# Performance work log

Hardware: AMD Instinct MI355X
Metric: run time of the kernel (lower is better)

Reference implementation:

```python
import jax, jax.numpy as jnp
import numpy as np


def setup_inputs() -> dict:
    key = jax.random.key(0)
    k1, k2 = jax.random.split(key)
    B, C, H, W = 8, 256, 128, 128
    x = jax.random.normal(k1, (B, C, H, W), dtype=jnp.float32)
    # prior plays the role of torch.rand initial selection score (shape [B, H*W])
    prior = jax.random.uniform(k2, (B, H * W), dtype=jnp.float32)
    return {"x": x, "prior": prior, "nbVec": 16}


def reference(x, prior, nbVec):
    # representativeVectors(x, nbVec, prior=prior, onlySimSample=True, applyUMAP=False)
    B, C, H, W = x.shape
    N = H * W
    xf = x.transpose(0, 2, 3, 1).reshape(B, N, C)  # [B, N, C]
    batch = jnp.arange(B)
    EPS = 1e-12  # numerical guard for sqrt at the selected point (dist == 0)

    def step(carry, i):
        score, selpos = carry  # score: [B, N] selection score, selpos: [B, N]
        # i == 0: deterministic center pick; else data-dependent argmax of score
        ind = jnp.where(i == 0, N // 2, jnp.argmax(score, axis=1))  # [B]
        selpos = selpos.at[batch, ind].add(1.0)
        rv = xf[batch, ind]  # gathered representative candidates [B, C]
        # exp(-euclidean_dist / 20) similarity to every spatial position
        d = jnp.sqrt(jnp.sum((xf - rv[:, None, :]) ** 2, axis=-1) + EPS)  # [B, N]
        sim = jnp.exp(-d / 20.0)
        simNorm = sim / jnp.sum(sim, axis=1, keepdims=True)
        repr_vec = jnp.einsum('bnc,bn->bc', xf, simNorm)  # weighted reduction
        score = jnp.where(i == 0, 1.0 - sim, (1.0 - sim) * score)
        return (score, selpos), (repr_vec, sim)

    init = (prior, jnp.zeros((B, N), dtype=x.dtype))
    (_, selpos), (reprVecs, sims) = jax.lax.scan(step, init, jnp.arange(nbVec))
    # reprVecs: [nbVec, B, C]; sims -> [nbVec, B, 1, H, W]; selpos -> [B, 1, H, W]
    return reprVecs, sims.reshape(nbVec, B, 1, H, W), selpos.reshape(B, 1, H, W)
```

## Files before the change

kernel.cpp:

```cpp
#include <hip/hip_runtime.h>
#include <math.h>

#define BB 8
#define CC 256
#define HH 128
#define WW 128
#define NN (HH*WW)
#define NBVEC 16
#define CSPLIT 16
#define CCHUNK (CC/CSPLIT)
#define NBX (NN/256)


__global__ __launch_bounds__(256, 8)
void fused_kernel(const float* __restrict__ x,
                  float* __restrict__ out,
                  const double* __restrict__ bmaxv,
                  const int* __restrict__ bmaxi,
                  double* __restrict__ d2part,
                  double* __restrict__ wpart, int iter)
{
    const int b  = blockIdx.z;
    const int cz = blockIdx.y;
    const int nb = blockIdx.x;
    const int t  = threadIdx.x;
    const int n  = nb*256 + t;

    __shared__ float s_x[CCHUNK][257];
    __shared__ float s_sim[256];
    __shared__ float s_rv[CCHUNK];
    __shared__ union UScratch {
        double part[16][CCHUNK];
        struct { double val[NBX]; int idx[NBX]; } mx;
    } s_u;

    float* out_sims   = out + (size_t)NBVEC*BB*CC;
    float* out_selpos = out_sims + (size_t)NBVEC*BB*NN;

    int sel = NN/2;
    if (iter > 0 && iter < NBVEC) {
        if (t < NBX) { s_u.mx.val[t] = bmaxv[b*NBX + t]; s_u.mx.idx[t] = bmaxi[b*NBX + t]; }
        __syncthreads();
        for (int s = NBX/2; s > 0; s >>= 1) {
            if (t < s) {
                double v2 = s_u.mx.val[t+s]; int i2 = s_u.mx.idx[t+s];
                if (v2 > s_u.mx.val[t] || (v2 == s_u.mx.val[t] && i2 < s_u.mx.idx[t])) {
                    s_u.mx.val[t] = v2; s_u.mx.idx[t] = i2;
                }
            }
            __syncthreads();
        }
        sel = s_u.mx.idx[0];
    }

    if (iter < NBVEC) {
        if (t < CCHUNK)
            s_rv[t] = x[((size_t)b*CC + (size_t)cz*CCHUNK + t)*NN + sel];
        if (t == 0 && nb == 0 && cz == 0)
            out_selpos[(size_t)b*NN + sel] += 1.0f;
    }
    if (iter > 0)
        s_sim[t] = out_sims[(size_t)(iter-1)*BB*NN + (size_t)b*NN + n];
    __syncthreads();

    const float* xb = x + ((size_t)b*CC + (size_t)cz*CCHUNK)*NN;
    float r[CCHUNK];
    #pragma unroll
    for (int c = 0; c < CCHUNK; ++c)
        r[c] = xb[(size_t)c*NN + n];
    #pragma unroll
    for (int c = 0; c < CCHUNK; ++c)
        s_x[c][t] = r[c];

    if (iter < NBVEC) {
        double acc = 0.0;
        #pragma unroll
        for (int c = 0; c < CCHUNK; ++c) {
            double diff = (double)r[c] - (double)s_rv[c];
            acc = fma(diff, diff, acc);
        }
        d2part[((size_t)cz*BB + b)*NN + n] = acc;
    }
    __syncthreads();

    if (iter > 0) {
        const int c = t & 15;
        const int g = t >> 4;
        double w = 0.0;
        #pragma unroll
        for (int k = 0; k < 16; ++k) {
            const int nn2 = g*16 + k;
            w = fma((double)s_sim[nn2], (double)s_x[c][nn2], w);
        }
        s_u.part[g][c] = w;
        __syncthreads();
        if (t < CCHUNK) {
            double tot = 0.0;
            #pragma unroll
            for (int gg = 0; gg < 16; ++gg) tot += s_u.part[gg][t];
            wpart[((size_t)nb*BB + b)*CC + (size_t)cz*CCHUNK + t] = tot;
        }
    }
}

__global__ void finish_kernel(float* __restrict__ out,
                              double* __restrict__ score,
                              const double* __restrict__ d2part,
                              double* __restrict__ sumSim,
                              const double* __restrict__ wpart,
                              double* __restrict__ bmaxv,
                              int* __restrict__ bmaxi, int iter)
{
    const int b = blockIdx.y;
    const int t = threadIdx.x;
    const int n = blockIdx.x * 256 + t;
    const size_t si = (size_t)b*NN + n;

    double d2 = 0.0;
    #pragma unroll
    for (int cz = 0; cz < CSPLIT; ++cz)
        d2 += d2part[((size_t)cz*BB + b)*NN + n];

    double d   = sqrt(d2 + 1e-12);
    double sim = exp(-(d / 20.0));

    float* out_sims = out + (size_t)NBVEC*BB*CC;
    out_sims[(size_t)iter*BB*NN + si] = (float)sim;

    double sc;
    if (iter == 0) sc = 1.0 - sim;
    else           sc = (1.0 - sim) * score[si];
    score[si] = sc;

    __shared__ double s_red[256];
    s_red[t] = sim;
    __syncthreads();
    for (int s = 128; s > 0; s >>= 1) {
        if (t < s) s_red[t] += s_red[t+s];
        __syncthreads();
    }
    if (t == 0) atomicAdd(&sumSim[(size_t)(iter & 1)*BB + b], s_red[0]);

    __shared__ double s_val[256];
    __shared__ int    s_idx[256];
    s_val[t] = sc; s_idx[t] = n;
    __syncthreads();
    for (int s = 128; s > 0; s >>= 1) {
        if (t < s) {
            double v2 = s_val[t+s]; int i2 = s_idx[t+s];
            if (v2 > s_val[t] || (v2 == s_val[t] && i2 < s_idx[t])) {
                s_val[t] = v2; s_idx[t] = i2;
            }
        }
        __syncthreads();
    }
    if (t == 0) {
        bmaxv[(size_t)b*NBX + blockIdx.x] = s_val[0];
        bmaxi[(size_t)b*NBX + blockIdx.x] = s_idx[0];
    }

    if (iter > 0 && blockIdx.x == 0) {
        const int slotPrev = (iter-1) & 1;
        double ss = sumSim[(size_t)slotPrev*BB + b];
        if (t < CC) {
            double tot = 0.0;
            for (int nb = 0; nb < NBX; ++nb)
                tot += wpart[((size_t)nb*BB + b)*CC + t];
            out[(size_t)(iter-1)*BB*CC + (size_t)b*CC + t] = (float)(tot / ss);
        }
        __syncthreads();
        if (t == 0) sumSim[(size_t)slotPrev*BB + b] = 0.0;
    }
}

__global__ void final_repr_kernel(float* __restrict__ out,
                                  const double* __restrict__ sumSim,
                                  const double* __restrict__ wpart)
{
    const int b = blockIdx.x;
    const int t = threadIdx.x;
    double ss = sumSim[(size_t)((NBVEC-1) & 1)*BB + b];
    if (t < CC) {
        double tot = 0.0;
        for (int nb = 0; nb < NBX; ++nb)
            tot += wpart[((size_t)nb*BB + b)*CC + t];
        out[(size_t)(NBVEC-1)*BB*CC + (size_t)b*CC + t] = (float)(tot / ss);
    }
}

extern "C" void kernel_launch(void* const* d_in, const int* in_sizes, int n_in,
                              void* d_out, int out_size, void* d_ws, size_t ws_size,
                              hipStream_t stream)
{
    const float* x = (const float*)d_in[0];
    float* out = (float*)d_out;

    char* ws = (char*)d_ws;
    double* score  = (double*)(ws);
    double* d2part = (double*)(ws + 1048576);
    double* wpart  = (double*)(ws + 17825792);
    double* sumSim = (double*)(ws + 18874368);
    double* bmaxv  = (double*)(ws + 18874496);
    int*    bmaxi  = (int*)   (ws + 18878592);

    float* out_selpos = out + (size_t)NBVEC*BB*CC + (size_t)NBVEC*BB*NN;
    hipMemsetAsync(out_selpos, 0, (size_t)BB*NN*sizeof(float), stream);
    hipMemsetAsync(sumSim, 0, 2*BB*sizeof(double), stream);

    for (int i = 0; i <= NBVEC; ++i) {
        fused_kernel<<<dim3(NBX, CSPLIT, BB), 256, 0, stream>>>(
            x, out, bmaxv, bmaxi, d2part, wpart, i);
        if (i < NBVEC)
            finish_kernel<<<dim3(NBX, BB), 256, 0, stream>>>(
                out, score, d2part, sumSim, wpart, bmaxv, bmaxi, i);
    }
    final_repr_kernel<<<BB, 256, 0, stream>>>(out, sumSim, wpart);
}
```

Measured before the change: 839.7 us.

## Store distance partials as float, use wave shuffle reductions, skip unneeded LDS staging

The per-channel-chunk squared-distance partials are now stored as float instead of double, halving the d2part write and read traffic between the fused and finish kernels. The finish kernel swaps its LDS tree reductions for the sum and argmax for 64-wide wave shuffles plus a small cross-wave step. The fused kernel skips writing x into shared memory on iteration 0, where it is not used. Several accumulation loops are split into multiple partial sums. Rounding the partials to float loses precision and could change argmax tie-breaking for near-equal scores.

```diff
diff --git a/kernel.cpp b/kernel.cpp
--- a/kernel.cpp
+++ b/kernel.cpp
@@ -17,7 +17,7 @@
                   float* __restrict__ out,
                   const double* __restrict__ bmaxv,
                   const int* __restrict__ bmaxi,
-                  double* __restrict__ d2part,
+                  float* __restrict__ d2part,
                   double* __restrict__ wpart, int iter)
 {
     const int b  = blockIdx.z;
@@ -68,9 +68,11 @@
     #pragma unroll
     for (int c = 0; c < CCHUNK; ++c)
         r[c] = xb[(size_t)c*NN + n];
-    #pragma unroll
-    for (int c = 0; c < CCHUNK; ++c)
-        s_x[c][t] = r[c];
+    if (iter > 0) {
+        #pragma unroll
+        for (int c = 0; c < CCHUNK; ++c)
+            s_x[c][t] = r[c];
+    }
 
     if (iter < NBVEC) {
         double acc = 0.0;
@@ -79,7 +81,7 @@
             double diff = (double)r[c] - (double)s_rv[c];
             acc = fma(diff, diff, acc);
         }
-        d2part[((size_t)cz*BB + b)*NN + n] = acc;
+        d2part[((size_t)cz*BB + b)*NN + n] = (float)acc;
     }
     __syncthreads();
 
@@ -95,17 +97,20 @@
         s_u.part[g][c] = w;
         __syncthreads();
         if (t < CCHUNK) {
-            double tot = 0.0;
+            double t0 = 0.0, t1 = 0.0;
             #pragma unroll
-            for (int gg = 0; gg < 16; ++gg) tot += s_u.part[gg][t];
-            wpart[((size_t)nb*BB + b)*CC + (size_t)cz*CCHUNK + t] = tot;
+            for (int gg = 0; gg < 16; gg += 2) {
+                t0 += s_u.part[gg][t];
+                t1 += s_u.part[gg+1][t];
+            }
+            wpart[((size_t)nb*BB + b)*CC + (size_t)cz*CCHUNK + t] = t0 + t1;
         }
     }
 }
 
 __global__ void finish_kernel(float* __restrict__ out,
                               double* __restrict__ score,
-                              const double* __restrict__ d2part,
+                              const float* __restrict__ d2part,
                               double* __restrict__ sumSim,
                               const double* __restrict__ wpart,
                               double* __restrict__ bmaxv,
@@ -115,11 +120,16 @@
     const int t = threadIdx.x;
     const int n = blockIdx.x * 256 + t;
     const size_t si = (size_t)b*NN + n;
-
-    double d2 = 0.0;
-    #pragma unroll
-    for (int cz = 0; cz < CSPLIT; ++cz)
-        d2 += d2part[((size_t)cz*BB + b)*NN + n];
+    const int lane = t & 63;
+    const int wave = t >> 6;
+
+    double a0 = 0.0, a1 = 0.0;
+    #pragma unroll
+    for (int cz = 0; cz < CSPLIT; cz += 2) {
+        a0 += (double)d2part[((size_t)cz*BB + b)*NN + n];
+        a1 += (double)d2part[((size_t)(cz+1)*BB + b)*NN + n];
+    }
+    double d2 = a0 + a1;
 
     double d   = sqrt(d2 + 1e-12);
     double sim = exp(-(d / 20.0));
@@ -132,40 +142,47 @@
     else           sc = (1.0 - sim) * score[si];
     score[si] = sc;
 
-    __shared__ double s_red[256];
-    s_red[t] = sim;
+    double v = sim;
+    #pragma unroll
+    for (int off = 32; off > 0; off >>= 1) v += __shfl_down(v, off, 64);
+
+    double bv = sc; int bi = n;
+    #pragma unroll
+    for (int off = 32; off > 0; off >>= 1) {
+        double ov = __shfl_down(bv, off, 64);
+        int    oi = __shfl_down(bi, off, 64);
+        if (ov > bv || (ov == bv && oi < bi)) { bv = ov; bi = oi; }
+    }
+
+    __shared__ double s_ws[4];
+    __shared__ double s_wv[4];
+    __shared__ int    s_wi[4];
+    if (lane == 0) { s_ws[wave] = v; s_wv[wave] = bv; s_wi[wave] = bi; }
     __syncthreads();
-    for (int s = 128; s > 0; s >>= 1) {
-        if (t < s) s_red[t] += s_red[t+s];
-        __syncthreads();
-    }
-    if (t == 0) atomicAdd(&sumSim[(size_t)(iter & 1)*BB + b], s_red[0]);
-
-    __shared__ double s_val[256];
-    __shared__ int    s_idx[256];
-    s_val[t] = sc; s_idx[t] = n;
-    __syncthreads();
-    for (int s = 128; s > 0; s >>= 1) {
-        if (t < s) {
-            double v2 = s_val[t+s]; int i2 = s_idx[t+s];
-            if (v2 > s_val[t] || (v2 == s_val[t] && i2 < s_idx[t])) {
-                s_val[t] = v2; s_idx[t] = i2;
-            }
-        }
-        __syncthreads();
-    }
     if (t == 0) {
-        bmaxv[(size_t)b*NBX + blockIdx.x] = s_val[0];
-        bmaxi[(size_t)b*NBX + blockIdx.x] = s_idx[0];
+        double tot = ((s_ws[0] + s_ws[1]) + (s_ws[2] + s_ws[3]));
+        atomicAdd(&sumSim[(size_t)(iter & 1)*BB + b], tot);
+        double cv = s_wv[0]; int ci = s_wi[0];
+        #pragma unroll
+        for (int w = 1; w < 4; ++w) {
+            if (s_wv[w] > cv || (s_wv[w] == cv && s_wi[w] < ci)) { cv = s_wv[w]; ci = s_wi[w]; }
+        }
+        bmaxv[(size_t)b*NBX + blockIdx.x] = cv;
+        bmaxi[(size_t)b*NBX + blockIdx.x] = ci;
     }
 
     if (iter > 0 && blockIdx.x == 0) {
         const int slotPrev = (iter-1) & 1;
         double ss = sumSim[(size_t)slotPrev*BB + b];
         if (t < CC) {
-            double tot = 0.0;
-            for (int nb = 0; nb < NBX; ++nb)
-                tot += wpart[((size_t)nb*BB + b)*CC + t];
+            double c0 = 0.0, c1 = 0.0, c2 = 0.0, c3 = 0.0;
+            for (int nb = 0; nb < NBX; nb += 4) {
+                c0 += wpart[((size_t)(nb+0)*BB + b)*CC + t];
+                c1 += wpart[((size_t)(nb+1)*BB + b)*CC + t];
+                c2 += wpart[((size_t)(nb+2)*BB + b)*CC + t];
+                c3 += wpart[((size_t)(nb+3)*BB + b)*CC + t];
+            }
+            double tot = ((c0 + c1) + (c2 + c3));
             out[(size_t)(iter-1)*BB*CC + (size_t)b*CC + t] = (float)(tot / ss);
         }
         __syncthreads();
@@ -181,9 +198,14 @@
     const int t = threadIdx.x;
     double ss = sumSim[(size_t)((NBVEC-1) & 1)*BB + b];
     if (t < CC) {
-        double tot = 0.0;
-        for (int nb = 0; nb < NBX; ++nb)
-            tot += wpart[((size_t)nb*BB + b)*CC + t];
+        double c0 = 0.0, c1 = 0.0, c2 = 0.0, c3 = 0.0;
+        for (int nb = 0; nb < NBX; nb += 4) {
+            c0 += wpart[((size_t)(nb+0)*BB + b)*CC + t];
+            c1 += wpart[((size_t)(nb+1)*BB + b)*CC + t];
+            c2 += wpart[((size_t)(nb+2)*BB + b)*CC + t];
+            c3 += wpart[((size_t)(nb+3)*BB + b)*CC + t];
+        }
+        double tot = ((c0 + c1) + (c2 + c3));
         out[(size_t)(NBVEC-1)*BB*CC + (size_t)b*CC + t] = (float)(tot / ss);
     }
 }
@@ -197,11 +219,11 @@
 
     char* ws = (char*)d_ws;
     double* score  = (double*)(ws);
-    double* d2part = (double*)(ws + 1048576);
-    double* wpart  = (double*)(ws + 17825792);
-    double* sumSim = (double*)(ws + 18874368);
-    double* bmaxv  = (double*)(ws + 18874496);
-    int*    bmaxi  = (int*)   (ws + 18878592);
+    float*  d2part = (float*) (ws + 1048576);
+    double* wpart  = (double*)(ws + 9437184);
+    double* sumSim = (double*)(ws + 10485760);
+    double* bmaxv  = (double*)(ws + 10485888);
+    int*    bmaxi  = (int*)   (ws + 10489984);
 
     float* out_selpos = out + (size_t)NBVEC*BB*CC + (size_t)NBVEC*BB*NN;
     hipMemsetAsync(out_selpos, 0, (size_t)BB*NN*sizeof(float), stream);
```

After: 861.4 us. 1.03x slower.
